# Performance work log

Measured on AMD Instinct MI355X. Metric: run time of the kernel, lower is better.

## Reference

```python
import jax, jax.numpy as jnp
import numpy as np

B, N, C = 4, 4096, 256  # batch, num_points, channels (in=out=key)
LN_EPS = 1e-6
STAB = 1e-9


def setup_inputs() -> dict:
    key = jax.random.key(0)
    ks = jax.random.split(key, 12)
    s = 0.02
    return {
        "inputs": jax.random.normal(ks[0], (B, N, C), jnp.float32),
        "mask": jax.random.randint(ks[1], (B, N), 0, 2).astype(bool),
        "Wq": s * jax.random.normal(ks[2], (C, C), jnp.float32),
        "bq": jnp.zeros((C,), jnp.float32),
        "Wk": s * jax.random.normal(ks[3], (C, C), jnp.float32),
        "bk": jnp.zeros((C,), jnp.float32),
        "Wv": s * jax.random.normal(ks[4], (C, C), jnp.float32),
        "bv": jnp.zeros((C,), jnp.float32),
        "Wo": s * jax.random.normal(ks[5], (C, C), jnp.float32),
        "bo": jnp.zeros((C,), jnp.float32),
        "ln_scale": jnp.ones((C,), jnp.float32),
        "ln_bias": jnp.zeros((C,), jnp.float32),
    }


def reference(inputs, mask, Wq, bq, Wk, bk, Wv, bv, Wo, bo, ln_scale, ln_bias):
    # kernel_size=1 Conv == pointwise dense
    q = inputs @ Wq + bq  # [B,N,C]
    k = inputs @ Wk + bk
    v = inputs @ Wv + bv
    att = jnp.einsum('bmc,bnc->bmn', q, k)  # [B,M,N]
    attn_mask = mask[:, :, None] & mask[:, None, :]  # make_attention_mask then squeeze
    big_neg = jnp.finfo(att.dtype).min
    att = jnp.where(attn_mask, att, big_neg)
    att = jax.nn.softmax(att, axis=-1)
    # extra renormalization over the M (query) axis
    att = att / (STAB + jnp.sum(att, axis=1, keepdims=True))
    # NOTE: faithful to source einsum '...MN,...NC->...NC' (sums over M only)
    out = jnp.einsum('bmn,bnc->bnc', att, v)  # [B,N,C]
    out = out @ Wo + bo
    # LayerNorm with reduction_axes=-2 (normalize over points axis)
    mean = jnp.mean(out, axis=-2, keepdims=True)
    var = jnp.mean(jnp.square(out), axis=-2, keepdims=True) - jnp.square(mean)
    out = (out - mean) * jax.lax.rsqrt(var + LN_EPS) * ln_scale + ln_bias
    out = jax.nn.relu(out)
    return out + inputs
```

## Files before the change

kernel.cpp:

```cpp
#include <hip/hip_runtime.h>
#include <math.h>

#define BATCH 4
#define NPTS 4096
#define CH 256
#define LN_EPS 1e-6f

typedef __attribute__((ext_vector_type(8))) _Float16 half8;
typedef __attribute__((ext_vector_type(4))) float f32x4;

__global__ __launch_bounds__(256) void fuse_weights(
    const float* __restrict__ Wv, const float* __restrict__ bv,
    const float* __restrict__ Wo, const float* __restrict__ bo,
    _Float16* __restrict__ Wct, float* __restrict__ bc,
    float* __restrict__ accg) {
    const int j = threadIdx.x;
    const int i = blockIdx.x;
    if (i < CH) {
        float acc = 0.f;
        #pragma unroll 4
        for (int c = 0; c < CH; c += 4) {
            const float4 wv = *(const float4*)&Wv[i * CH + c];
            acc = fmaf(wv.x, Wo[(c + 0) * CH + j], acc);
            acc = fmaf(wv.y, Wo[(c + 1) * CH + j], acc);
            acc = fmaf(wv.z, Wo[(c + 2) * CH + j], acc);
            acc = fmaf(wv.w, Wo[(c + 3) * CH + j], acc);
        }
        Wct[(size_t)j * CH + i] = (_Float16)acc;
    } else {
        float acc = bo[j];
        #pragma unroll 4
        for (int c = 0; c < CH; c += 4) {
            const float4 bv4 = *(const float4*)&bv[c];
            acc = fmaf(bv4.x, Wo[(c + 0) * CH + j], acc);
            acc = fmaf(bv4.y, Wo[(c + 1) * CH + j], acc);
            acc = fmaf(bv4.z, Wo[(c + 2) * CH + j], acc);
            acc = fmaf(bv4.w, Wo[(c + 3) * CH + j], acc);
        }
        bc[j] = acc;
        #pragma unroll
        for (int t = 0; t < 2 * BATCH; ++t)
            accg[t * CH + j] = 0.f;
    }
}

#define APAD 40
#define BPAD 264

__global__ __launch_bounds__(256) void gemm_fused(
    const float* __restrict__ A, const _Float16* __restrict__ Wct,
    const float* __restrict__ bc, float* __restrict__ u,
    float* __restrict__ accg) {
    __shared__ _Float16 Bst[64][BPAD];
    __shared__ _Float16 As[64][APAD];

    const int tid = threadIdx.x;
    const int m0 = blockIdx.x * 64;
    const int n0 = blockIdx.y * 64;
    const int w = tid >> 6;
    const int l = tid & 63;
    const int lr = l & 15;
    const int lq = l >> 4;

    {
        const int nr = tid >> 2;
        const int ks = (tid & 3) * 64;
        #pragma unroll
        for (int i = 0; i < 8; ++i) {
            half8 v = *(const half8*)&Wct[(size_t)(n0 + nr) * CH + ks + i * 8];
            *(half8*)&Bst[nr][ks + i * 8] = v;
        }
    }

    f32x4 acc[4];
    #pragma unroll
    for (int f = 0; f < 4; ++f) acc[f] = (f32x4){0.f, 0.f, 0.f, 0.f};

    const int arow = tid >> 2;
    const int akseg = (tid & 3) * 8;

    for (int kc = 0; kc < CH; kc += 32) {
        const float* aptr = &A[(size_t)(m0 + arow) * CH + kc + akseg];
        const float4 a0 = *(const float4*)aptr;
        const float4 a1 = *(const float4*)(aptr + 4);
        half8 ah;
        ah[0] = (_Float16)a0.x; ah[1] = (_Float16)a0.y;
        ah[2] = (_Float16)a0.z; ah[3] = (_Float16)a0.w;
        ah[4] = (_Float16)a1.x; ah[5] = (_Float16)a1.y;
        ah[6] = (_Float16)a1.z; ah[7] = (_Float16)a1.w;

        __syncthreads();
        *(half8*)&As[arow][akseg] = ah;
        __syncthreads();

        const half8 afrag = *(const half8*)&As[w * 16 + lr][lq * 8];
        #pragma unroll
        for (int f = 0; f < 4; ++f) {
            const half8 bfrag = *(const half8*)&Bst[f * 16 + lr][kc + lq * 8];
            acc[f] = __builtin_amdgcn_mfma_f32_16x16x32_f16(afrag, bfrag, acc[f], 0, 0, 0);
        }
    }

    const int batch = m0 >> 12;
    const int mbase = m0 + w * 16 + lq * 4;
    #pragma unroll
    for (int f = 0; f < 4; ++f) {
        const int n = n0 + f * 16 + lr;
        const float bcn = bc[n];
        float s1 = 0.f, s2 = 0.f;
        #pragma unroll
        for (int r = 0; r < 4; ++r) {
            const float v = acc[f][r] + bcn;
            u[(size_t)(mbase + r) * CH + n] = v;
            s1 += v;
            s2 = fmaf(v, v, s2);
        }
        s1 += __shfl_xor(s1, 16, 64);
        s1 += __shfl_xor(s1, 32, 64);
        s2 += __shfl_xor(s2, 16, 64);
        s2 += __shfl_xor(s2, 32, 64);
        if (lq == 0) {
            atomicAdd(&accg[batch * CH + n], s1);
            atomicAdd(&accg[BATCH * CH + batch * CH + n], s2);
        }
    }
}

__global__ __launch_bounds__(256) void ln_finish(
    const float* __restrict__ u, const float* __restrict__ inp,
    const float* __restrict__ accg, const float* __restrict__ scale,
    const float* __restrict__ bias, float* __restrict__ out) {
    const int idx = blockIdx.x * blockDim.x + threadIdx.x;
    const int c4 = (idx & 63) * 4;
    const int bn = idx >> 6;
    const int b = bn >> 12;
    const size_t off = (size_t)idx * 4;

    const float4 uv = *(const float4*)&u[off];
    const float4 xv = *(const float4*)&inp[off];
    const float4 s1 = *(const float4*)&accg[b * CH + c4];
    const float4 s2 = *(const float4*)&accg[BATCH * CH + b * CH + c4];
    const float4 sc = *(const float4*)&scale[c4];
    const float4 bi = *(const float4*)&bias[c4];

    const float invN = 1.f / (float)NPTS;
    float uu[4] = {uv.x, uv.y, uv.z, uv.w};
    float xx[4] = {xv.x, xv.y, xv.z, xv.w};
    float a1[4] = {s1.x, s1.y, s1.z, s1.w};
    float a2[4] = {s2.x, s2.y, s2.z, s2.w};
    float scv[4] = {sc.x, sc.y, sc.z, sc.w};
    float biv[4] = {bi.x, bi.y, bi.z, bi.w};
    float r[4];
    #pragma unroll
    for (int j = 0; j < 4; ++j) {
        const float mean = a1[j] * invN;
        const float var = a2[j] * invN - mean * mean;
        const float inv = rsqrtf(var + LN_EPS);
        float y = (uu[j] - mean) * inv * scv[j] + biv[j];
        r[j] = fmaxf(y, 0.f) + xx[j];
    }
    float4 ro;
    ro.x = r[0]; ro.y = r[1]; ro.z = r[2]; ro.w = r[3];
    *(float4*)&out[off] = ro;
}

extern "C" void kernel_launch(void* const* d_in, const int* in_sizes, int n_in,
                              void* d_out, int out_size, void* d_ws, size_t ws_size,
                              hipStream_t stream) {
    const float* inputs   = (const float*)d_in[0];
    const float* Wv       = (const float*)d_in[6];
    const float* bv       = (const float*)d_in[7];
    const float* Wo       = (const float*)d_in[8];
    const float* bo       = (const float*)d_in[9];
    const float* ln_scale = (const float*)d_in[10];
    const float* ln_bias  = (const float*)d_in[11];
    float* out = (float*)d_out;

    float*     u    = (float*)d_ws;
    float*     accg = (float*)((char*)d_ws + (size_t)BATCH * NPTS * CH * 4);
    _Float16*  Wct  = (_Float16*)((char*)accg + 2 * BATCH * CH * 4);
    float*     bc   = (float*)((char*)Wct + (size_t)CH * CH * 2);

    fuse_weights<<<CH + 1, 256, 0, stream>>>(Wv, bv, Wo, bo, Wct, bc, accg);
    gemm_fused<<<dim3((BATCH * NPTS) / 64, CH / 64), 256, 0, stream>>>(
        inputs, Wct, bc, u, accg);
    ln_finish<<<(BATCH * NPTS * CH / 4) / 256, 256, 0, stream>>>(
        u, inputs, accg, ln_scale, ln_bias, out);
}
```

Baseline: 121.6 us.

## Fuse GEMM and LayerNorm finish via cooperative grid sync, keeping results in registers

```diff
diff --git a/kernel.cpp b/kernel.cpp
--- a/kernel.cpp
+++ b/kernel.cpp
@@ -1,4 +1,5 @@
 #include <hip/hip_runtime.h>
+#include <hip/hip_cooperative_groups.h>
 #include <math.h>
 
 #define BATCH 4
@@ -47,121 +48,128 @@
 #define APAD 40
 #define BPAD 264
 
-__global__ __launch_bounds__(256) void gemm_fused(
+__global__ __launch_bounds__(256, 2) void gemm_ln_fused(
     const float* __restrict__ A, const _Float16* __restrict__ Wct,
-    const float* __restrict__ bc, float* __restrict__ u,
-    float* __restrict__ accg) {
+    const float* __restrict__ bc, float* __restrict__ accg,
+    const float* __restrict__ scale, const float* __restrict__ bias,
+    float* __restrict__ out) {
     __shared__ _Float16 Bst[64][BPAD];
     __shared__ _Float16 As[64][APAD];
+    __shared__ float sstats[2][2][64];
 
     const int tid = threadIdx.x;
-    const int m0 = blockIdx.x * 64;
-    const int n0 = blockIdx.y * 64;
+    const int nt = blockIdx.x >> 7;
+    const int mti = blockIdx.x & 127;
+    const int n0 = nt * 64;
     const int w = tid >> 6;
     const int l = tid & 63;
     const int lr = l & 15;
     const int lq = l >> 4;
+    const int m0t[2] = {mti * 64, (mti + 128) * 64};
 
     {
         const int nr = tid >> 2;
         const int ks = (tid & 3) * 64;
         #pragma unroll
-        for (int i = 0; i < 8; ++i) {
-            half8 v = *(const half8*)&Wct[(size_t)(n0 + nr) * CH + ks + i * 8];
-            *(half8*)&Bst[nr][ks + i * 8] = v;
-        }
+        for (int i = 0; i < 8; ++i)
+            *(half8*)&Bst[nr][ks + i * 8] =
+                *(const half8*)&Wct[(size_t)(n0 + nr) * CH + ks + i * 8];
     }
 
-    f32x4 acc[4];
+    f32x4 acc[2][4];
     #pragma unroll
-    for (int f = 0; f < 4; ++f) acc[f] = (f32x4){0.f, 0.f, 0.f, 0.f};
+    for (int t = 0; t < 2; ++t)
+        #pragma unroll
+        for (int f = 0; f < 4; ++f) acc[t][f] = (f32x4){0.f, 0.f, 0.f, 0.f};
 
     const int arow = tid >> 2;
     const int akseg = (tid & 3) * 8;
 
-    for (int kc = 0; kc < CH; kc += 32) {
-        const float* aptr = &A[(size_t)(m0 + arow) * CH + kc + akseg];
-        const float4 a0 = *(const float4*)aptr;
-        const float4 a1 = *(const float4*)(aptr + 4);
-        half8 ah;
-        ah[0] = (_Float16)a0.x; ah[1] = (_Float16)a0.y;
-        ah[2] = (_Float16)a0.z; ah[3] = (_Float16)a0.w;
-        ah[4] = (_Float16)a1.x; ah[5] = (_Float16)a1.y;
-        ah[6] = (_Float16)a1.z; ah[7] = (_Float16)a1.w;
+    #pragma unroll 1
+    for (int t = 0; t < 2; ++t) {
+        const int m0 = m0t[t];
+        for (int kc = 0; kc < CH; kc += 32) {
+            const float* aptr = &A[(size_t)(m0 + arow) * CH + kc + akseg];
+            const float4 a0 = *(const float4*)aptr;
+            const float4 a1 = *(const float4*)(aptr + 4);
+            half8 ah;
+            ah[0] = (_Float16)a0.x; ah[1] = (_Float16)a0.y;
+            ah[2] = (_Float16)a0.z; ah[3] = (_Float16)a0.w;
+            ah[4] = (_Float16)a1.x; ah[5] = (_Float16)a1.y;
+            ah[6] = (_Float16)a1.z; ah[7] = (_Float16)a1.w;
 
-        __syncthreads();
-        *(half8*)&As[arow][akseg] = ah;
-        __syncthreads();
+            __syncthreads();
+            *(half8*)&As[arow][akseg] = ah;
+            __syncthreads();
 
-        const half8 afrag = *(const half8*)&As[w * 16 + lr][lq * 8];
-        #pragma unroll
-        for (int f = 0; f < 4; ++f) {
-            const half8 bfrag = *(const half8*)&Bst[f * 16 + lr][kc + lq * 8];
-            acc[f] = __builtin_amdgcn_mfma_f32_16x16x32_f16(afrag, bfrag, acc[f], 0, 0, 0);
+            const half8 afrag = *(const half8*)&As[w * 16 + lr][lq * 8];
+            #pragma unroll
+            for (int f = 0; f < 4; ++f) {
+                const half8 bfrag = *(const half8*)&Bst[f * 16 + lr][kc + lq * 8];
+                acc[t][f] = __builtin_amdgcn_mfma_f32_16x16x32_f16(
+                    afrag, bfrag, acc[t][f], 0, 0, 0);
+            }
         }
     }
 
-    const int batch = m0 >> 12;
-    const int mbase = m0 + w * 16 + lq * 4;
     #pragma unroll
-    for (int f = 0; f < 4; ++f) {
-        const int n = n0 + f * 16 + lr;
-        const float bcn = bc[n];
-        float s1 = 0.f, s2 = 0.f;
+    for (int t = 0; t < 2; ++t) {
+        const int batch = m0t[t] >> 12;
         #pragma unroll
-        for (int r = 0; r < 4; ++r) {
-            const float v = acc[f][r] + bcn;
-            u[(size_t)(mbase + r) * CH + n] = v;
-            s1 += v;
-            s2 = fmaf(v, v, s2);
-        }
-        s1 += __shfl_xor(s1, 16, 64);
-        s1 += __shfl_xor(s1, 32, 64);
-        s2 += __shfl_xor(s2, 16, 64);
-        s2 += __shfl_xor(s2, 32, 64);
-        if (lq == 0) {
-            atomicAdd(&accg[batch * CH + n], s1);
-            atomicAdd(&accg[BATCH * CH + batch * CH + n], s2);
+        for (int f = 0; f < 4; ++f) {
+            const int n = n0 + f * 16 + lr;
+            const float bcn = bc[n];
+            float s1 = 0.f, s2 = 0.f;
+            #pragma unroll
+            for (int r = 0; r < 4; ++r) {
+                const float v = acc[t][f][r] + bcn;
+                acc[t][f][r] = v;
+                s1 += v;
+                s2 = fmaf(v, v, s2);
+            }
+            s1 += __shfl_xor(s1, 16, 64);
+            s1 += __shfl_xor(s1, 32, 64);
+            s2 += __shfl_xor(s2, 16, 64);
+            s2 += __shfl_xor(s2, 32, 64);
+            if (lq == 0) {
+                atomicAdd(&accg[batch * CH + n], s1);
+                atomicAdd(&accg[BATCH * CH + batch * CH + n], s2);
+            }
         }
     }
-}
 
-__global__ __launch_bounds__(256) void ln_finish(
-    const float* __restrict__ u, const float* __restrict__ inp,
-    const float* __restrict__ accg, const float* __restrict__ scale,
-    const float* __restrict__ bias, float* __restrict__ out) {
-    const int idx = blockIdx.x * blockDim.x + threadIdx.x;
-    const int c4 = (idx & 63) * 4;
-    const int bn = idx >> 6;
-    const int b = bn >> 12;
-    const size_t off = (size_t)idx * 4;
+    cooperative_groups::this_grid().sync();
 
-    const float4 uv = *(const float4*)&u[off];
-    const float4 xv = *(const float4*)&inp[off];
-    const float4 s1 = *(const float4*)&accg[b * CH + c4];
-    const float4 s2 = *(const float4*)&accg[BATCH * CH + b * CH + c4];
-    const float4 sc = *(const float4*)&scale[c4];
-    const float4 bi = *(const float4*)&bias[c4];
+    {
+        const int t = tid >> 7;
+        const int s = (tid >> 6) & 1;
+        const int nl = tid & 63;
+        const int batch = m0t[t] >> 12;
+        sstats[t][s][nl] = accg[s * BATCH * CH + batch * CH + n0 + nl];
+    }
+    __syncthreads();
 
     const float invN = 1.f / (float)NPTS;
-    float uu[4] = {uv.x, uv.y, uv.z, uv.w};
-    float xx[4] = {xv.x, xv.y, xv.z, xv.w};
-    float a1[4] = {s1.x, s1.y, s1.z, s1.w};
-    float a2[4] = {s2.x, s2.y, s2.z, s2.w};
-    float scv[4] = {sc.x, sc.y, sc.z, sc.w};
-    float biv[4] = {bi.x, bi.y, bi.z, bi.w};
-    float r[4];
     #pragma unroll
-    for (int j = 0; j < 4; ++j) {
-        const float mean = a1[j] * invN;
-        const float var = a2[j] * invN - mean * mean;
-        const float inv = rsqrtf(var + LN_EPS);
-        float y = (uu[j] - mean) * inv * scv[j] + biv[j];
-        r[j] = fmaxf(y, 0.f) + xx[j];
+    for (int t = 0; t < 2; ++t) {
+        const int mb = m0t[t] + w * 16 + lq * 4;
+        #pragma unroll
+        for (int f = 0; f < 4; ++f) {
+            const int nl = f * 16 + lr;
+            const int n = n0 + nl;
+            const float mean = sstats[t][0][nl] * invN;
+            const float var = sstats[t][1][nl] * invN - mean * mean;
+            const float inv = rsqrtf(var + LN_EPS);
+            const float sc = scale[n] * inv;
+            const float bi = bias[n];
+            #pragma unroll
+            for (int r = 0; r < 4; ++r) {
+                const size_t off = (size_t)(mb + r) * CH + n;
+                const float y = fmaxf((acc[t][f][r] - mean) * sc + bi, 0.f);
+                out[off] = y + A[off];
+            }
+        }
     }
-    float4 ro;
-    ro.x = r[0]; ro.y = r[1]; ro.z = r[2]; ro.w = r[3];
-    *(float4*)&out[off] = ro;
 }
 
 extern "C" void kernel_launch(void* const* d_in, const int* in_sizes, int n_in,
@@ -176,14 +184,14 @@
     const float* ln_bias  = (const float*)d_in[11];
     float* out = (float*)d_out;
 
-    float*     u    = (float*)d_ws;
-    float*     accg = (float*)((char*)d_ws + (size_t)BATCH * NPTS * CH * 4);
-    _Float16*  Wct  = (_Float16*)((char*)accg + 2 * BATCH * CH * 4);
-    float*     bc   = (float*)((char*)Wct + (size_t)CH * CH * 2);
+    float*    accg = (float*)d_ws;
+    _Float16* Wct  = (_Float16*)((char*)accg + 2 * BATCH * CH * 4);
+    float*    bc   = (float*)((char*)Wct + (size_t)CH * CH * 2);
 
     fuse_weights<<<CH + 1, 256, 0, stream>>>(Wv, bv, Wo, bo, Wct, bc, accg);
-    gemm_fused<<<dim3((BATCH * NPTS) / 64, CH / 64), 256, 0, stream>>>(
-        inputs, Wct, bc, u, accg);
-    ln_finish<<<(BATCH * NPTS * CH / 4) / 256, 256, 0, stream>>>(
-        u, inputs, accg, ln_scale, ln_bias, out);
+
+    void* args[] = {(void*)&inputs, (void*)&Wct, (void*)&bc, (void*)&accg,
+                    (void*)&ln_scale, (void*)&ln_bias, (void*)&out};
+    hipLaunchCooperativeKernel((const void*)gemm_ln_fused, dim3(512), dim3(256),
+                               args, 0, stream);
 }
```

Measured after the change: 248.1 us. 104% more time.
